# Optimization experiments

Measured on AMD Instinct MI355X. Metric: run time of the kernel, lower is better.

The kernel has to match this reference:

```python
import jax, jax.numpy as jnp
import numpy as np

DIM = 64
K = 7
GC = 8            # groups_channels (hardcoded in module)
G = DIM // GC     # groups = 8
RED = 2           # reduction_ratio
PAD = (K - 1) // 2


def _patches(y, k, p):
    # torch nn.Unfold(k, dilation=1, padding=p, stride=1) ordering: (c, kh, kw)
    b, c, H, W = y.shape
    yp = jnp.pad(y, ((0, 0), (0, 0), (p, p), (p, p)))
    tiles = [yp[:, :, i:i + H, j:j + W] for i in range(k) for j in range(k)]
    return jnp.stack(tiles, axis=2)  # (b, c, k*k, H, W)


def setup_inputs() -> dict:
    key = jax.random.key(0)
    ks = jax.random.split(key, 6)
    b, h, w = 4, 128, 128
    input_x = jax.random.normal(ks[0], (b, DIM, h, w), dtype=jnp.float32)
    input_y = jax.random.normal(ks[1], (b, DIM, h, w), dtype=jnp.float32)
    c_mid = DIM // RED
    w1 = jax.random.normal(ks[2], (c_mid, DIM), dtype=jnp.float32) * 0.05
    b1 = jnp.zeros((c_mid,), dtype=jnp.float32)
    w2 = jax.random.normal(ks[3], (K * K * G, c_mid), dtype=jnp.float32) * 0.05
    b2 = jnp.zeros((K * K * G,), dtype=jnp.float32)
    return {"input_x": input_x, "input_y": input_y, "w1": w1, "b1": b1, "w2": w2, "b2": b2}


def reference(input_x, input_y, w1, b1, w2, b2):
    b, c, h, w = input_x.shape
    # 1x1 convs generating dynamic kernels (stride == 1, no avgpool)
    mid = jnp.einsum('bchw,oc->bohw', input_x, w1) + b1[None, :, None, None]
    weight = jnp.einsum('bchw,oc->bohw', mid, w2) + b2[None, :, None, None]
    # (b, G, 1, k*k, h, w) broadcast over groups_channels
    weight = weight.reshape(b, G, K * K, h, w)[:, :, None]
    # unfold input_y -> (b, G, GC, k*k, h, w)
    out = _patches(input_y, K, PAD).reshape(b, G, GC, K * K, h, w)
    out = (weight * out).sum(axis=3).reshape(b, DIM, h, w)
    return out
```

## Files before the change

### kernel.cpp

```cpp
#include <hip/hip_runtime.h>
#include <hip/hip_fp16.h>

#define DIMC 64
#define KS 7
#define NTAP 49
#define GCH 8
#define NG 8
#define CMID 32
#define PADD 3
#define HH 128
#define WW 128
#define PLANE (HH*WW)
#define TW 32
#define TH 8
#define TPX (TW+2*PADD)
#define TPY (TH+2*PADD)
#define NPIX (TPX*TPY)
#define NB 4
#define WTSTR 36
#define CPAD 12

#define WC_OFF 0
#define BC_OFF 65536
#define XT_OFF 67584
#define Y16_OFF (XT_OFF + 8388608)
#define WS_NEED ((size_t)Y16_OFF + 8388608)

typedef __attribute__((ext_vector_type(8))) short short8;
typedef __attribute__((ext_vector_type(4))) float f32x4;
typedef __fp16 fp16x2 __attribute__((ext_vector_type(2)));

static __device__ inline unsigned short f2bs(float f) {
    union { float f; unsigned u; } v; v.f = f;
    unsigned r = v.u + 0x7fff + ((v.u >> 16) & 1);
    return (unsigned short)(r >> 16);
}

static __device__ inline unsigned pkh(float a, float b) {
    union { fp16x2 h; unsigned u; } c;
    c.h = __builtin_amdgcn_cvt_pkrtz(a, b);
    return c.u;
}

__global__ __launch_bounds__(256)
void prep_all(const float* __restrict__ x, const float* __restrict__ y,
              const float* __restrict__ w1, const float* __restrict__ b1,
              const float* __restrict__ w2, const float* __restrict__ b2,
              unsigned short* __restrict__ wc, float* __restrict__ bc,
              unsigned short* __restrict__ xt, unsigned short* __restrict__ y16) {
    const int bid = blockIdx.x;
    if (bid < 1024) {
        const int bid2 = bid & 511;
        const int pxblk = bid2 & 63, rest = bid2 >> 6;
        const int b = rest & 3, h = rest >> 2;
        const int px = pxblk * 256 + threadIdx.x;
        const float* sp = ((bid < 512) ? x : y) + (size_t)b * DIMC * PLANE + (size_t)h * 32 * PLANE + px;
        unsigned short* dp = (bid < 512) ? xt : y16;
        const bool isx = (bid < 512);
        #pragma unroll
        for (int q = 0; q < 4; ++q) {
            unsigned pk[4];
            #pragma unroll
            for (int j = 0; j < 4; ++j) {
                float v0 = sp[(size_t)(q * 8 + 2 * j) * PLANE];
                float v1 = sp[(size_t)(q * 8 + 2 * j + 1) * PLANE];
                pk[j] = isx ? (((unsigned)f2bs(v1) << 16) | f2bs(v0)) : pkh(v0, v1);
            }
            *reinterpret_cast<uint4*>(dp + (((size_t)b * 8 + h * 4 + q) * PLANE + px) * 8) =
                make_uint4(pk[0], pk[1], pk[2], pk[3]);
        }
    } else {
        const int idx = (bid - 1024) * 256 + threadIdx.x;
        const int row64 = idx >> 4;
        const int c0 = (idx & 15) * 4;
        const int g = row64 >> 6, r = row64 & 63;
        float a0 = 0.f, a1 = 0.f, a2 = 0.f, a3 = 0.f, bv = 0.f;
        if (r < NTAP) {
            const float* w2r = w2 + (g * NTAP + r) * CMID;
            #pragma unroll
            for (int m = 0; m < CMID; ++m) {
                float wv = w2r[m];
                const float* w1r = w1 + m * DIMC + c0;
                a0 = fmaf(wv, w1r[0], a0);
                a1 = fmaf(wv, w1r[1], a1);
                a2 = fmaf(wv, w1r[2], a2);
                a3 = fmaf(wv, w1r[3], a3);
            }
            if (c0 == 0) {
                bv = b2[g * NTAP + r];
                #pragma unroll
                for (int m = 0; m < CMID; ++m) bv = fmaf(w2r[m], b1[m], bv);
            }
        }
        *reinterpret_cast<uint2*>(wc + row64 * DIMC + c0) =
            make_uint2(((unsigned)f2bs(a1) << 16) | f2bs(a0),
                       ((unsigned)f2bs(a3) << 16) | f2bs(a2));
        if ((idx & 15) == 0) bc[row64] = bv;
    }
}

__global__ __launch_bounds__(256, 4)
void invol_mfma8_kernel(const unsigned short* __restrict__ y16,
                        const unsigned short* __restrict__ xt,
                        const unsigned short* __restrict__ wc,
                        const float* __restrict__ bc,
                        float* __restrict__ out) {
    __shared__ __half ytile[NPIX * GCH];
    __shared__ __half wtl[256 * WTSTR];

    const int tid = threadIdx.x;
    const int l = tid & 63, w = tid >> 6;
    const int fr = l & 15, fk = l >> 4;
    const int bx = blockIdx.x, by = blockIdx.y;
    const int b = blockIdx.z >> 3, g = blockIdx.z & 7;
    const int tx = tid & 31, ty = tid >> 5;

    int gpix[4];
    #pragma unroll
    for (int nt = 0; nt < 4; ++nt) {
        int lp = w * 64 + nt * 16 + fr;
        gpix[nt] = (by * TH + (lp >> 5)) * WW + bx * TW + (lp & 31);
    }
    short8 bf[2][4];
    #pragma unroll
    for (int kp = 0; kp < 2; ++kp)
        #pragma unroll
        for (int nt = 0; nt < 4; ++nt) {
            union { uint4 u; short8 s; } cv;
            cv.u = *reinterpret_cast<const uint4*>(
                xt + (((size_t)b * 8 + kp * 4 + fk) * PLANE + gpix[nt]) * 8);
            bf[kp][nt] = cv.s;
        }
    short8 af[4][2];
    #pragma unroll
    for (int dmt = 0; dmt < 4; ++dmt)
        #pragma unroll
        for (int kp = 0; kp < 2; ++kp) {
            union { uint4 u; short8 s; } cv;
            cv.u = *reinterpret_cast<const uint4*>(
                wc + ((size_t)(g * 64 + dmt * 16 + fr)) * DIMC + kp * 32 + fk * 8);
            af[dmt][kp] = cv.s;
        }

    const unsigned short* y16g = y16 + ((size_t)(b * 8 + g) * PLANE) * 8;
    #pragma unroll
    for (int k = 0; k < 3; ++k) {
        int i = tid + k * 256;
        if (i < NPIX) {
            int r = i / TPX, col = i - r * TPX;
            int sy = by * TH + r - PADD, sx = bx * TW + col - PADD;
            bool ok = (sy >= 0 && sy < HH && sx >= 0 && sx < WW);
            uint4 v = make_uint4(0u, 0u, 0u, 0u);
            if (ok) v = *reinterpret_cast<const uint4*>(y16g + (size_t)(sy * WW + sx) * 8);
            *reinterpret_cast<uint4*>(&ytile[i * GCH]) = v;
        }
    }

    __syncthreads();

    __half2 acch[4];
    #pragma unroll
    for (int cc = 0; cc < 4; ++cc) acch[cc] = __float2half2_rn(0.f);
    const int ybase = (ty * TPX + tx) * GCH;

    #pragma unroll
    for (int mc = 0; mc < 2; ++mc) {
        f32x4 acc[2][4];
        #pragma unroll
        for (int dm = 0; dm < 2; ++dm)
            #pragma unroll
            for (int nt = 0; nt < 4; ++nt)
                acc[dm][nt] = f32x4{0.f, 0.f, 0.f, 0.f};

        #pragma unroll
        for (int dm = 0; dm < 2; ++dm)
            #pragma unroll
            for (int kp = 0; kp < 2; ++kp)
                #pragma unroll
                for (int nt = 0; nt < 4; ++nt)
                    acc[dm][nt] = __builtin_amdgcn_mfma_f32_16x16x32_bf16(
                        af[mc * 2 + dm][kp], bf[kp][nt], acc[dm][nt], 0, 0, 0);

        #pragma unroll
        for (int dm = 0; dm < 2; ++dm) {
            int rb = (mc * 2 + dm) * 16 + fk * 4;
            float4 bb = *reinterpret_cast<const float4*>(&bc[g * 64 + rb]);
            #pragma unroll
            for (int nt = 0; nt < 4; ++nt) {
                int lp = w * 64 + nt * 16 + fr;
                *reinterpret_cast<uint2*>(&wtl[lp * WTSTR + dm * 16 + fk * 4]) =
                    make_uint2(pkh(acc[dm][nt][0] + bb.x, acc[dm][nt][1] + bb.y),
                               pkh(acc[dm][nt][2] + bb.z, acc[dm][nt][3] + bb.w));
            }
        }

        uint2 wr[8];
        #pragma unroll
        for (int q = 0; q < 8; ++q)
            wr[q] = *reinterpret_cast<const uint2*>(&wtl[tid * WTSTR + q * 4]);

        const int ninv = (mc == 0) ? 32 : 17;
        #pragma unroll
        for (int j = 0; j < 32; ++j) {
            if (j >= ninv) break;
            const int kk = mc * 32 + j;
            const int ky = kk / 7, kx = kk - ky * 7;
            unsigned uh = (j & 2) ? wr[j >> 2].y : wr[j >> 2].x;
            union { unsigned u; __half2 h; } hc; hc.u = uh;
            __half wh = (j & 1) ? __high2half(hc.h) : __low2half(hc.h);
            __half2 wv2 = __half2half2(wh);
            union { uint4 u; __half2 h[4]; } yvv;
            yvv.u = *reinterpret_cast<const uint4*>(&ytile[ybase + (ky * TPX + kx) * GCH]);
            acch[0] = __hfma2(wv2, yvv.h[0], acch[0]);
            acch[1] = __hfma2(wv2, yvv.h[1], acch[1]);
            acch[2] = __hfma2(wv2, yvv.h[2], acch[2]);
            acch[3] = __hfma2(wv2, yvv.h[3], acch[3]);
        }
    }

    const int gy = by * TH + ty, gx = bx * TW + tx;
    float* op = out + ((size_t)(b * DIMC + g * GCH) * HH + gy) * WW + gx;
    #pragma unroll
    for (int cc = 0; cc < 4; ++cc) {
        float2 f = __half22float2(acch[cc]);
        op[(2 * cc) * PLANE]     = f.x;
        op[(2 * cc + 1) * PLANE] = f.y;
    }
}

__global__ __launch_bounds__(256, 1)
void invol_fused_kernel(const float* __restrict__ x, const float* __restrict__ y,
                        const float* __restrict__ w1, const float* __restrict__ b1,
                        const float* __restrict__ w2, const float* __restrict__ b2,
                        float* __restrict__ out) {
    __shared__ float ytile[NPIX * CPAD];
    const int tid = threadIdx.x;
    const int tx = tid & 31, ty = tid >> 5;
    const int bx = blockIdx.x, by = blockIdx.y, bz = blockIdx.z;
    const int gx = bx * TW + tx, gy = by * TH + ty;

    float xv[DIMC];
    const float* xp = x + ((size_t)(bz * DIMC) * HH + gy) * WW + gx;
    #pragma unroll
    for (int c = 0; c < DIMC; ++c) xv[c] = xp[c * PLANE];

    float mid[CMID];
    #pragma unroll
    for (int m = 0; m < CMID; ++m) {
        float a = b1[m];
        const float4* w1r = reinterpret_cast<const float4*>(w1 + m * DIMC);
        #pragma unroll
        for (int cq = 0; cq < DIMC / 4; ++cq) {
            float4 wv = w1r[cq];
            a = fmaf(wv.x, xv[4*cq+0], a);
            a = fmaf(wv.y, xv[4*cq+1], a);
            a = fmaf(wv.z, xv[4*cq+2], a);
            a = fmaf(wv.w, xv[4*cq+3], a);
        }
        mid[m] = a;
    }

    for (int g = 0; g < NG; ++g) {
        __syncthreads();
        for (int i = tid; i < NPIX * GCH; i += 256) {
            int c = i / NPIX;
            int p = i - c * NPIX;
            int r = p / TPX;
            int col = p - r * TPX;
            int sy = by * TH + r - PADD;
            int sx = bx * TW + col - PADD;
            float v = 0.f;
            if (sy >= 0 && sy < HH && sx >= 0 && sx < WW)
                v = y[((size_t)(bz * DIMC + g * GCH + c) * HH + sy) * WW + sx];
            ytile[p * CPAD + c] = v;
        }
        __syncthreads();

        float wt[NTAP];
        const float*  b2g = b2 + g * NTAP;
        const float4* w2g = reinterpret_cast<const float4*>(w2 + g * NTAP * CMID);
        #pragma unroll
        for (int kk = 0; kk < NTAP; ++kk) {
            float a = b2g[kk];
            #pragma unroll
            for (int mq = 0; mq < CMID / 4; ++mq) {
                float4 wv = w2g[kk * (CMID / 4) + mq];
                a = fmaf(wv.x, mid[4*mq+0], a);
                a = fmaf(wv.y, mid[4*mq+1], a);
                a = fmaf(wv.z, mid[4*mq+2], a);
                a = fmaf(wv.w, mid[4*mq+3], a);
            }
            wt[kk] = a;
        }

        float acc[GCH];
        #pragma unroll
        for (int cc = 0; cc < GCH; ++cc) acc[cc] = 0.f;
        #pragma unroll
        for (int ky = 0; ky < KS; ++ky) {
            #pragma unroll
            for (int kx = 0; kx < KS; ++kx) {
                float wv = wt[ky * KS + kx];
                int pp = (ty + ky) * TPX + (tx + kx);
                const float4* yr = reinterpret_cast<const float4*>(&ytile[pp * CPAD]);
                float4 ya = yr[0];
                float4 yb = yr[1];
                acc[0] = fmaf(wv, ya.x, acc[0]);
                acc[1] = fmaf(wv, ya.y, acc[1]);
                acc[2] = fmaf(wv, ya.z, acc[2]);
                acc[3] = fmaf(wv, ya.w, acc[3]);
                acc[4] = fmaf(wv, yb.x, acc[4]);
                acc[5] = fmaf(wv, yb.y, acc[5]);
                acc[6] = fmaf(wv, yb.z, acc[6]);
                acc[7] = fmaf(wv, yb.w, acc[7]);
            }
        }

        float* op = out + ((size_t)(bz * DIMC + g * GCH) * HH + gy) * WW + gx;
        #pragma unroll
        for (int cc = 0; cc < GCH; ++cc) op[cc * PLANE] = acc[cc];
    }
}

extern "C" void kernel_launch(void* const* d_in, const int* in_sizes, int n_in,
                              void* d_out, int out_size, void* d_ws, size_t ws_size,
                              hipStream_t stream) {
    const float* x  = (const float*)d_in[0];
    const float* y  = (const float*)d_in[1];
    const float* w1 = (const float*)d_in[2];
    const float* b1 = (const float*)d_in[3];
    const float* w2 = (const float*)d_in[4];
    const float* b2 = (const float*)d_in[5];
    float* out = (float*)d_out;

    if (ws_size >= WS_NEED) {
        char* ws = (char*)d_ws;
        unsigned short* wcp  = (unsigned short*)(ws + WC_OFF);
        float*          bcp  = (float*)(ws + BC_OFF);
        unsigned short* xtp  = (unsigned short*)(ws + XT_OFF);
        unsigned short* y16p = (unsigned short*)(ws + Y16_OFF);

        hipLaunchKernelGGL(prep_all, dim3(1024 + 32), dim3(256), 0, stream,
                           x, y, w1, b1, w2, b2, wcp, bcp, xtp, y16p);
        hipLaunchKernelGGL(invol_mfma8_kernel, dim3(WW / TW, HH / TH, NB * NG), dim3(256), 0, stream,
                           y16p, xtp, wcp, bcp, out);
    } else {
        dim3 grid(WW / TW, HH / TH, NB);
        hipLaunchKernelGGL(invol_fused_kernel, grid, dim3(256), 0, stream,
                           x, y, w1, b1, w2, b2, out);
    }
}
```

Before: 34.19 us.

## Fuse input precision conversion into main kernel, drop intermediate bf16/fp16 buffers

Removes the prep pass that converted x and y into packed bf16/fp16 channel-interleaved workspace buffers. The main kernel now reads the fp32 inputs directly and converts them in registers: x goes into bf16 MFMA B fragments, and y goes into the fp16 LDS tile as two 4-channel halves. This saves a full read and write of both inputs through global memory. In exchange, each block reads fp32 data with strided per-channel loads. The x features are also re-read once per group block (8 times across the grid), which raises global traffic.

```diff
diff --git a/kernel.cpp b/kernel.cpp
--- a/kernel.cpp
+++ b/kernel.cpp
@@ -22,9 +22,7 @@
 
 #define WC_OFF 0
 #define BC_OFF 65536
-#define XT_OFF 67584
-#define Y16_OFF (XT_OFF + 8388608)
-#define WS_NEED ((size_t)Y16_OFF + 8388608)
+#define WS_NEED ((size_t)BC_OFF + 2048)
 
 typedef __attribute__((ext_vector_type(8))) short short8;
 typedef __attribute__((ext_vector_type(4))) float f32x4;
@@ -43,65 +41,39 @@
 }
 
 __global__ __launch_bounds__(256)
-void prep_all(const float* __restrict__ x, const float* __restrict__ y,
-              const float* __restrict__ w1, const float* __restrict__ b1,
-              const float* __restrict__ w2, const float* __restrict__ b2,
-              unsigned short* __restrict__ wc, float* __restrict__ bc,
-              unsigned short* __restrict__ xt, unsigned short* __restrict__ y16) {
-    const int bid = blockIdx.x;
-    if (bid < 1024) {
-        const int bid2 = bid & 511;
-        const int pxblk = bid2 & 63, rest = bid2 >> 6;
-        const int b = rest & 3, h = rest >> 2;
-        const int px = pxblk * 256 + threadIdx.x;
-        const float* sp = ((bid < 512) ? x : y) + (size_t)b * DIMC * PLANE + (size_t)h * 32 * PLANE + px;
-        unsigned short* dp = (bid < 512) ? xt : y16;
-        const bool isx = (bid < 512);
-        #pragma unroll
-        for (int q = 0; q < 4; ++q) {
-            unsigned pk[4];
-            #pragma unroll
-            for (int j = 0; j < 4; ++j) {
-                float v0 = sp[(size_t)(q * 8 + 2 * j) * PLANE];
-                float v1 = sp[(size_t)(q * 8 + 2 * j + 1) * PLANE];
-                pk[j] = isx ? (((unsigned)f2bs(v1) << 16) | f2bs(v0)) : pkh(v0, v1);
-            }
-            *reinterpret_cast<uint4*>(dp + (((size_t)b * 8 + h * 4 + q) * PLANE + px) * 8) =
-                make_uint4(pk[0], pk[1], pk[2], pk[3]);
-        }
-    } else {
-        const int idx = (bid - 1024) * 256 + threadIdx.x;
-        const int row64 = idx >> 4;
-        const int c0 = (idx & 15) * 4;
-        const int g = row64 >> 6, r = row64 & 63;
-        float a0 = 0.f, a1 = 0.f, a2 = 0.f, a3 = 0.f, bv = 0.f;
-        if (r < NTAP) {
-            const float* w2r = w2 + (g * NTAP + r) * CMID;
-            #pragma unroll
-            for (int m = 0; m < CMID; ++m) {
-                float wv = w2r[m];
-                const float* w1r = w1 + m * DIMC + c0;
-                a0 = fmaf(wv, w1r[0], a0);
-                a1 = fmaf(wv, w1r[1], a1);
-                a2 = fmaf(wv, w1r[2], a2);
-                a3 = fmaf(wv, w1r[3], a3);
-            }
-            if (c0 == 0) {
-                bv = b2[g * NTAP + r];
-                #pragma unroll
-                for (int m = 0; m < CMID; ++m) bv = fmaf(w2r[m], b1[m], bv);
-            }
-        }
-        *reinterpret_cast<uint2*>(wc + row64 * DIMC + c0) =
-            make_uint2(((unsigned)f2bs(a1) << 16) | f2bs(a0),
-                       ((unsigned)f2bs(a3) << 16) | f2bs(a2));
-        if ((idx & 15) == 0) bc[row64] = bv;
-    }
+void prep_wc(const float* __restrict__ w1, const float* __restrict__ b1,
+             const float* __restrict__ w2, const float* __restrict__ b2,
+             unsigned short* __restrict__ wc, float* __restrict__ bc) {
+    const int idx = blockIdx.x * 256 + threadIdx.x;
+    const int row64 = idx >> 4;
+    const int c0 = (idx & 15) * 4;
+    const int g = row64 >> 6, r = row64 & 63;
+    float a0 = 0.f, a1 = 0.f, a2 = 0.f, a3 = 0.f, bv = 0.f;
+    if (r < NTAP) {
+        const float* w2r = w2 + (g * NTAP + r) * CMID;
+        #pragma unroll
+        for (int m = 0; m < CMID; ++m) {
+            float wv = w2r[m];
+            const float* w1r = w1 + m * DIMC + c0;
+            a0 = fmaf(wv, w1r[0], a0);
+            a1 = fmaf(wv, w1r[1], a1);
+            a2 = fmaf(wv, w1r[2], a2);
+            a3 = fmaf(wv, w1r[3], a3);
+        }
+        if (c0 == 0) {
+            bv = b2[g * NTAP + r];
+            #pragma unroll
+            for (int m = 0; m < CMID; ++m) bv = fmaf(w2r[m], b1[m], bv);
+        }
+    }
+    *reinterpret_cast<uint2*>(wc + row64 * DIMC + c0) =
+        make_uint2(((unsigned)f2bs(a1) << 16) | f2bs(a0),
+                   ((unsigned)f2bs(a3) << 16) | f2bs(a2));
+    if ((idx & 15) == 0) bc[row64] = bv;
 }
 
 __global__ __launch_bounds__(256, 4)
-void invol_mfma8_kernel(const unsigned short* __restrict__ y16,
-                        const unsigned short* __restrict__ xt,
+void invol_mfma9_kernel(const float* __restrict__ x, const float* __restrict__ y,
                         const unsigned short* __restrict__ wc,
                         const float* __restrict__ bc,
                         float* __restrict__ out) {
@@ -121,16 +93,26 @@
         int lp = w * 64 + nt * 16 + fr;
         gpix[nt] = (by * TH + (lp >> 5)) * WW + bx * TW + (lp & 31);
     }
+
+    const float* xb = x + (size_t)b * DIMC * PLANE;
     short8 bf[2][4];
     #pragma unroll
     for (int kp = 0; kp < 2; ++kp)
         #pragma unroll
         for (int nt = 0; nt < 4; ++nt) {
+            const float* xp = xb + (size_t)(kp * 32 + fk * 8) * PLANE + gpix[nt];
+            unsigned d[4];
+            #pragma unroll
+            for (int jj = 0; jj < 4; ++jj) {
+                float v0 = xp[(size_t)(2 * jj) * PLANE];
+                float v1 = xp[(size_t)(2 * jj + 1) * PLANE];
+                d[jj] = ((unsigned)f2bs(v1) << 16) | f2bs(v0);
+            }
             union { uint4 u; short8 s; } cv;
-            cv.u = *reinterpret_cast<const uint4*>(
-                xt + (((size_t)b * 8 + kp * 4 + fk) * PLANE + gpix[nt]) * 8);
+            cv.u = make_uint4(d[0], d[1], d[2], d[3]);
             bf[kp][nt] = cv.s;
         }
+
     short8 af[4][2];
     #pragma unroll
     for (int dmt = 0; dmt < 4; ++dmt)
@@ -142,17 +124,23 @@
             af[dmt][kp] = cv.s;
         }
 
-    const unsigned short* y16g = y16 + ((size_t)(b * 8 + g) * PLANE) * 8;
-    #pragma unroll
-    for (int k = 0; k < 3; ++k) {
+    const float* yg = y + (size_t)(b * DIMC + g * GCH) * PLANE;
+    #pragma unroll
+    for (int k = 0; k < 5; ++k) {
         int i = tid + k * 256;
-        if (i < NPIX) {
-            int r = i / TPX, col = i - r * TPX;
+        if (i < NPIX * 2) {
+            int q  = i / NPIX;
+            int px = i - q * NPIX;
+            int r = px / TPX, col = px - r * TPX;
             int sy = by * TH + r - PADD, sx = bx * TW + col - PADD;
             bool ok = (sy >= 0 && sy < HH && sx >= 0 && sx < WW);
-            uint4 v = make_uint4(0u, 0u, 0u, 0u);
-            if (ok) v = *reinterpret_cast<const uint4*>(y16g + (size_t)(sy * WW + sx) * 8);
-            *reinterpret_cast<uint4*>(&ytile[i * GCH]) = v;
+            const float* yp = yg + (size_t)(q * 4) * PLANE + sy * WW + sx;
+            float v0 = ok ? yp[0] : 0.f;
+            float v1 = ok ? yp[PLANE] : 0.f;
+            float v2 = ok ? yp[2 * PLANE] : 0.f;
+            float v3 = ok ? yp[3 * PLANE] : 0.f;
+            *reinterpret_cast<uint2*>(&ytile[px * GCH + q * 4]) =
+                make_uint2(pkh(v0, v1), pkh(v2, v3));
         }
     }
 
@@ -335,15 +323,13 @@
 
     if (ws_size >= WS_NEED) {
         char* ws = (char*)d_ws;
-        unsigned short* wcp  = (unsigned short*)(ws + WC_OFF);
-        float*          bcp  = (float*)(ws + BC_OFF);
-        unsigned short* xtp  = (unsigned short*)(ws + XT_OFF);
-        unsigned short* y16p = (unsigned short*)(ws + Y16_OFF);
-
-        hipLaunchKernelGGL(prep_all, dim3(1024 + 32), dim3(256), 0, stream,
-                           x, y, w1, b1, w2, b2, wcp, bcp, xtp, y16p);
-        hipLaunchKernelGGL(invol_mfma8_kernel, dim3(WW / TW, HH / TH, NB * NG), dim3(256), 0, stream,
-                           y16p, xtp, wcp, bcp, out);
+        unsigned short* wcp = (unsigned short*)(ws + WC_OFF);
+        float*          bcp = (float*)(ws + BC_OFF);
+
+        hipLaunchKernelGGL(prep_wc, dim3(32), dim3(256), 0, stream,
+                           w1, b1, w2, b2, wcp, bcp);
+        hipLaunchKernelGGL(invol_mfma9_kernel, dim3(WW / TW, HH / TH, NB * NG), dim3(256), 0, stream,
+                           x, y, wcp, bcp, out);
     } else {
         dim3 grid(WW / TW, HH / TH, NB);
         hipLaunchKernelGGL(invol_fused_kernel, grid, dim3(256), 0, stream,
```

Result: slower. 36.55 us (+6.9%).

## Process two groups per block to reuse loaded x-tile fragments

Applied to the files above, without the earlier changes.

Each block now handles two involution groups instead of one, halving the grid. The bf fragments (x projected through w1) loaded from global memory are shared across both groups, so xt is read half as often. Both y tiles are staged into shared memory up front, and the second group's weight fragments are loaded mid-computation. The cost is more shared memory and registers per block, which may lower occupancy, and half as many blocks to spread across the GPU.

```diff
diff --git a/kernel.cpp b/kernel.cpp
--- a/kernel.cpp
+++ b/kernel.cpp
@@ -100,19 +100,19 @@
 }
 
 __global__ __launch_bounds__(256, 4)
-void invol_mfma8_kernel(const unsigned short* __restrict__ y16,
-                        const unsigned short* __restrict__ xt,
-                        const unsigned short* __restrict__ wc,
-                        const float* __restrict__ bc,
-                        float* __restrict__ out) {
-    __shared__ __half ytile[NPIX * GCH];
+void invol_mfma12_kernel(const unsigned short* __restrict__ y16,
+                         const unsigned short* __restrict__ xt,
+                         const unsigned short* __restrict__ wc,
+                         const float* __restrict__ bc,
+                         float* __restrict__ out) {
+    __shared__ __half ytile[2][NPIX * GCH];
     __shared__ __half wtl[256 * WTSTR];
 
     const int tid = threadIdx.x;
     const int l = tid & 63, w = tid >> 6;
     const int fr = l & 15, fk = l >> 4;
     const int bx = blockIdx.x, by = blockIdx.y;
-    const int b = blockIdx.z >> 3, g = blockIdx.z & 7;
+    const int b = blockIdx.z >> 2, g0 = (blockIdx.z & 3) * 2;
     const int tx = tid & 31, ty = tid >> 5;
 
     int gpix[4];
@@ -131,100 +131,120 @@
                 xt + (((size_t)b * 8 + kp * 4 + fk) * PLANE + gpix[nt]) * 8);
             bf[kp][nt] = cv.s;
         }
-    short8 af[4][2];
+    short8 af[2][4][2];
     #pragma unroll
     for (int dmt = 0; dmt < 4; ++dmt)
         #pragma unroll
         for (int kp = 0; kp < 2; ++kp) {
             union { uint4 u; short8 s; } cv;
             cv.u = *reinterpret_cast<const uint4*>(
-                wc + ((size_t)(g * 64 + dmt * 16 + fr)) * DIMC + kp * 32 + fk * 8);
-            af[dmt][kp] = cv.s;
-        }
-
-    const unsigned short* y16g = y16 + ((size_t)(b * 8 + g) * PLANE) * 8;
-    #pragma unroll
-    for (int k = 0; k < 3; ++k) {
+                wc + ((size_t)(g0 * 64 + dmt * 16 + fr)) * DIMC + kp * 32 + fk * 8);
+            af[0][dmt][kp] = cv.s;
+        }
+
+    #pragma unroll
+    for (int k = 0; k < 5; ++k) {
         int i = tid + k * 256;
-        if (i < NPIX) {
-            int r = i / TPX, col = i - r * TPX;
+        if (i < NPIX * 2) {
+            int gg = i / NPIX;
+            int px = i - gg * NPIX;
+            int r = px / TPX, col = px - r * TPX;
             int sy = by * TH + r - PADD, sx = bx * TW + col - PADD;
             bool ok = (sy >= 0 && sy < HH && sx >= 0 && sx < WW);
             uint4 v = make_uint4(0u, 0u, 0u, 0u);
-            if (ok) v = *reinterpret_cast<const uint4*>(y16g + (size_t)(sy * WW + sx) * 8);
-            *reinterpret_cast<uint4*>(&ytile[i * GCH]) = v;
+            if (ok) v = *reinterpret_cast<const uint4*>(
+                y16 + (((size_t)(b * 8 + g0 + gg) * PLANE) + (size_t)(sy * WW + sx)) * 8);
+            *reinterpret_cast<uint4*>(&ytile[gg][px * GCH]) = v;
         }
     }
 
     __syncthreads();
 
-    __half2 acch[4];
-    #pragma unroll
-    for (int cc = 0; cc < 4; ++cc) acch[cc] = __float2half2_rn(0.f);
     const int ybase = (ty * TPX + tx) * GCH;
-
-    #pragma unroll
-    for (int mc = 0; mc < 2; ++mc) {
-        f32x4 acc[2][4];
-        #pragma unroll
-        for (int dm = 0; dm < 2; ++dm)
-            #pragma unroll
-            for (int nt = 0; nt < 4; ++nt)
-                acc[dm][nt] = f32x4{0.f, 0.f, 0.f, 0.f};
-
-        #pragma unroll
-        for (int dm = 0; dm < 2; ++dm)
-            #pragma unroll
-            for (int kp = 0; kp < 2; ++kp)
+    const int gy = by * TH + ty, gx = bx * TW + tx;
+
+    #pragma unroll
+    for (int gg = 0; gg < 2; ++gg) {
+        const int g = g0 + gg;
+
+        __half2 acch[4];
+        #pragma unroll
+        for (int cc = 0; cc < 4; ++cc) acch[cc] = __float2half2_rn(0.f);
+
+        #pragma unroll
+        for (int mc = 0; mc < 2; ++mc) {
+            f32x4 acc[2][4];
+            #pragma unroll
+            for (int dm = 0; dm < 2; ++dm)
                 #pragma unroll
                 for (int nt = 0; nt < 4; ++nt)
-                    acc[dm][nt] = __builtin_amdgcn_mfma_f32_16x16x32_bf16(
-                        af[mc * 2 + dm][kp], bf[kp][nt], acc[dm][nt], 0, 0, 0);
-
-        #pragma unroll
-        for (int dm = 0; dm < 2; ++dm) {
-            int rb = (mc * 2 + dm) * 16 + fk * 4;
-            float4 bb = *reinterpret_cast<const float4*>(&bc[g * 64 + rb]);
-            #pragma unroll
-            for (int nt = 0; nt < 4; ++nt) {
-                int lp = w * 64 + nt * 16 + fr;
-                *reinterpret_cast<uint2*>(&wtl[lp * WTSTR + dm * 16 + fk * 4]) =
-                    make_uint2(pkh(acc[dm][nt][0] + bb.x, acc[dm][nt][1] + bb.y),
-                               pkh(acc[dm][nt][2] + bb.z, acc[dm][nt][3] + bb.w));
-            }
-        }
-
-        uint2 wr[8];
-        #pragma unroll
-        for (int q = 0; q < 8; ++q)
-            wr[q] = *reinterpret_cast<const uint2*>(&wtl[tid * WTSTR + q * 4]);
-
-        const int ninv = (mc == 0) ? 32 : 17;
-        #pragma unroll
-        for (int j = 0; j < 32; ++j) {
-            if (j >= ninv) break;
-            const int kk = mc * 32 + j;
-            const int ky = kk / 7, kx = kk - ky * 7;
-            unsigned uh = (j & 2) ? wr[j >> 2].y : wr[j >> 2].x;
-            union { unsigned u; __half2 h; } hc; hc.u = uh;
-            __half wh = (j & 1) ? __high2half(hc.h) : __low2half(hc.h);
-            __half2 wv2 = __half2half2(wh);
-            union { uint4 u; __half2 h[4]; } yvv;
-            yvv.u = *reinterpret_cast<const uint4*>(&ytile[ybase + (ky * TPX + kx) * GCH]);
-            acch[0] = __hfma2(wv2, yvv.h[0], acch[0]);
-            acch[1] = __hfma2(wv2, yvv.h[1], acch[1]);
-            acch[2] = __hfma2(wv2, yvv.h[2], acch[2]);
-            acch[3] = __hfma2(wv2, yvv.h[3], acch[3]);
-        }
-    }
-
-    const int gy = by * TH + ty, gx = bx * TW + tx;
-    float* op = out + ((size_t)(b * DIMC + g * GCH) * HH + gy) * WW + gx;
-    #pragma unroll
-    for (int cc = 0; cc < 4; ++cc) {
-        float2 f = __half22float2(acch[cc]);
-        op[(2 * cc) * PLANE]     = f.x;
-        op[(2 * cc + 1) * PLANE] = f.y;
+                    acc[dm][nt] = f32x4{0.f, 0.f, 0.f, 0.f};
+
+            #pragma unroll
+            for (int dm = 0; dm < 2; ++dm)
+                #pragma unroll
+                for (int kp = 0; kp < 2; ++kp)
+                    #pragma unroll
+                    for (int nt = 0; nt < 4; ++nt)
+                        acc[dm][nt] = __builtin_amdgcn_mfma_f32_16x16x32_bf16(
+                            af[gg][mc * 2 + dm][kp], bf[kp][nt], acc[dm][nt], 0, 0, 0);
+
+            #pragma unroll
+            for (int dm = 0; dm < 2; ++dm) {
+                int rb = (mc * 2 + dm) * 16 + fk * 4;
+                float4 bb = *reinterpret_cast<const float4*>(&bc[g * 64 + rb]);
+                #pragma unroll
+                for (int nt = 0; nt < 4; ++nt) {
+                    int lp = w * 64 + nt * 16 + fr;
+                    *reinterpret_cast<uint2*>(&wtl[lp * WTSTR + dm * 16 + fk * 4]) =
+                        make_uint2(pkh(acc[dm][nt][0] + bb.x, acc[dm][nt][1] + bb.y),
+                                   pkh(acc[dm][nt][2] + bb.z, acc[dm][nt][3] + bb.w));
+                }
+            }
+
+            if (gg == 0 && mc == 0) {
+                #pragma unroll
+                for (int dmt = 0; dmt < 4; ++dmt)
+                    #pragma unroll
+                    for (int kp = 0; kp < 2; ++kp) {
+                        union { uint4 u; short8 s; } cv;
+                        cv.u = *reinterpret_cast<const uint4*>(
+                            wc + ((size_t)((g0 + 1) * 64 + dmt * 16 + fr)) * DIMC + kp * 32 + fk * 8);
+                        af[1][dmt][kp] = cv.s;
+                    }
+            }
+
+            uint2 wr[8];
+            #pragma unroll
+            for (int q = 0; q < 8; ++q)
+                wr[q] = *reinterpret_cast<const uint2*>(&wtl[tid * WTSTR + q * 4]);
+
+            const int ninv = (mc == 0) ? 32 : 17;
+            #pragma unroll
+            for (int j = 0; j < 32; ++j) {
+                if (j >= ninv) break;
+                const int kk = mc * 32 + j;
+                const int ky = kk / 7, kx = kk - ky * 7;
+                unsigned uh = (j & 2) ? wr[j >> 2].y : wr[j >> 2].x;
+                union { unsigned u; __half2 h; } hc; hc.u = uh;
+                __half wh = (j & 1) ? __high2half(hc.h) : __low2half(hc.h);
+                __half2 wv2 = __half2half2(wh);
+                union { uint4 u; __half2 h[4]; } yvv;
+                yvv.u = *reinterpret_cast<const uint4*>(&ytile[gg][ybase + (ky * TPX + kx) * GCH]);
+                acch[0] = __hfma2(wv2, yvv.h[0], acch[0]);
+                acch[1] = __hfma2(wv2, yvv.h[1], acch[1]);
+                acch[2] = __hfma2(wv2, yvv.h[2], acch[2]);
+                acch[3] = __hfma2(wv2, yvv.h[3], acch[3]);
+            }
+        }
+
+        float* op = out + ((size_t)(b * DIMC + g * GCH) * HH + gy) * WW + gx;
+        #pragma unroll
+        for (int cc = 0; cc < 4; ++cc) {
+            float2 f = __half22float2(acch[cc]);
+            op[(2 * cc) * PLANE]     = f.x;
+            op[(2 * cc + 1) * PLANE] = f.y;
+        }
     }
 }
 
@@ -342,7 +362,7 @@
 
         hipLaunchKernelGGL(prep_all, dim3(1024 + 32), dim3(256), 0, stream,
                            x, y, w1, b1, w2, b2, wcp, bcp, xtp, y16p);
-        hipLaunchKernelGGL(invol_mfma8_kernel, dim3(WW / TW, HH / TH, NB * NG), dim3(256), 0, stream,
+        hipLaunchKernelGGL(invol_mfma12_kernel, dim3(WW / TW, HH / TH, NB * NG / 2), dim3(256), 0, stream,
                            y16p, xtp, wcp, bcp, out);
     } else {
         dim3 grid(WW / TW, HH / TH, NB);
```

Measured after the change: 44.43 us. +29.9%, slower.
